# Kernel optimization log

Measured on AMD Instinct MI355X. Metric: run time of the kernel, lower is better.

The kernel has to match this reference:

```python
import jax, jax.numpy as jnp
import numpy as np
from math import sqrt

B, L, S, H, E = 4, 2048, 2048, 8, 64
T = 1.0  # softmax temperature


def setup_inputs() -> dict:
    key = jax.random.key(0)
    kq, kk, kv = jax.random.split(key, 3)
    q = jax.random.normal(kq, (B, L, H, E), dtype=jnp.float32)
    k = jax.random.normal(kk, (B, S, H, E), dtype=jnp.float32)
    v = jax.random.normal(kv, (B, S, H, E), dtype=jnp.float32)
    mask = jnp.zeros((B, L), dtype=jnp.bool_)  # unused by the module, kept for signature fidelity
    return {"q": q, "k": k, "v": v, "mask": mask}


def reference(q, k, v, mask):
    Bq, Lq, Hq, Eq = q.shape
    # [B,L,H,E] -> [B,H,E,L]; FFT over time axis
    xq = jnp.transpose(q, (0, 2, 3, 1))
    xk = jnp.transpose(k, (0, 2, 3, 1))
    xv = jnpp_t = jnp.transpose(v, (0, 2, 3, 1))
    xq_ft = jnp.fft.rfft(xq, axis=-1, norm='ortho')   # [B,H,E,Lf]
    xk_ft = jnp.fft.rfft(xk, axis=-1, norm='ortho')   # [B,H,E,Sf]
    xv_ft = jnp.fft.rfft(xv, axis=-1, norm='ortho')   # [B,H,E,Sf]
    # complex frequency-domain scores [B,H,Lf,Sf]
    scores = jnp.einsum('bhex,bhey->bhxy', xq_ft, jnp.conj(xk_ft)) / sqrt(Eq)
    # activation == 'softmax': softmax over |scores|/T, then real-weighted complex mix
    attn = jax.nn.softmax(jnp.abs(scores) / T, axis=-1)
    xqkv_ft = jnp.einsum('bhxy,bhey->bhex', attn.astype(xv_ft.dtype), xv_ft)  # [B,H,E,Lf]
    out = jnp.fft.irfft(xqkv_ft, n=Lq, axis=-1, norm='ortho')  # [B,H,E,L]
    return jnp.transpose(out, (0, 3, 1, 2))  # [B,L,H,E]
```

## Files before the change

kernel.cpp:

```cpp
#include <hip/hip_runtime.h>
#include <hip/hip_bf16.h>
#include <math.h>

#define LOGN  11
#define NN    2048
#define LOGM  10
#define MM    1024
#define NF    1025
#define NYP   1056
#define TWO_PI 6.283185307179586f
#define INV_SQRT_N 0.022097086912079608f
#define INV_SCALE  0.044194173824159216f
#define LOG2E      1.4426950408889634f

#define PAD(i) ((i) + ((i) >> 4))
#define MMP   1088
#define TWP   816

typedef __attribute__((ext_vector_type(8))) short bhalf8;
typedef __attribute__((ext_vector_type(4))) float f32x4;

#define MFMA16(a, b, c) __builtin_amdgcn_mfma_f32_16x16x32_bf16(a, b, c, 0, 0, 0)

#define GLD16(gp, lp)                                                              \
    __builtin_amdgcn_global_load_lds(                                              \
        (const __attribute__((address_space(1))) void*)(gp),                       \
        (__attribute__((address_space(3))) void*)(lp), 16, 0, 0)

#define CVTPK(dst, lo, hi) \
    asm("v_cvt_pk_bf16_f32 %0, %1, %2" : "=v"(dst) : "v"(lo), "v"(hi))

#define EXP2F(dst, src) \
    asm("v_exp_f32 %0, %1" : "=v"(dst) : "v"(src))

__device__ __forceinline__ unsigned short f2bf(float f) {
    union { float f; unsigned u; } v; v.f = f;
    unsigned r = v.u + 0x7FFFu + ((v.u >> 16) & 1u);
    return (unsigned short)(r >> 16);
}
__device__ __forceinline__ float bf2f(unsigned short h) {
    union { unsigned u; float f; } v; v.u = ((unsigned)h) << 16;
    return v.f;
}

__device__ __forceinline__ int dr4_10(unsigned j) {
    unsigned r = __brev(j) >> 22;
    return (int)(((r & 0x155u) << 1) | ((r >> 1) & 0x155u));
}

__global__ __launch_bounds__(256) void mk_tables(float2* __restrict__ twf,
                                                 float2* __restrict__ twi,
                                                 float2* __restrict__ rc)
{
    int i = blockIdx.x * 256 + threadIdx.x;
    if (i < 768) {
        float ang = TWO_PI * (float)i / (float)MM;
        float sv, cv;
        __sincosf(ang, &sv, &cv);
        twf[i] = make_float2(cv, -sv);
        twi[i] = make_float2(cv,  sv);
    }
    if (i < 1025) {
        float ang = TWO_PI * (float)i / (float)NN;
        float sv, cv;
        __sincosf(ang, &sv, &cv);
        rc[i] = make_float2(cv, sv);
    }
}

template<bool FWD>
__device__ __forceinline__ void fft_r4_1024(float2* buf, const float2* tw, int tid)
{
    {
        int i0 = tid * 4;
        int q0 = PAD(i0), q1 = PAD(i0 + 1), q2 = PAD(i0 + 2), q3 = PAD(i0 + 3);
        float2 a = buf[q0], b = buf[q1], c = buf[q2], d = buf[q3];
        float2 apc = make_float2(a.x + c.x, a.y + c.y);
        float2 amc = make_float2(a.x - c.x, a.y - c.y);
        float2 bpd = make_float2(b.x + d.x, b.y + d.y);
        float2 bmd = make_float2(b.x - d.x, b.y - d.y);
        buf[q0] = make_float2(apc.x + bpd.x, apc.y + bpd.y);
        buf[q2] = make_float2(apc.x - bpd.x, apc.y - bpd.y);
        if (FWD) {
            buf[q1] = make_float2(amc.x + bmd.y, amc.y - bmd.x);
            buf[q3] = make_float2(amc.x - bmd.y, amc.y + bmd.x);
        } else {
            buf[q1] = make_float2(amc.x - bmd.y, amc.y + bmd.x);
            buf[q3] = make_float2(amc.x + bmd.y, amc.y - bmd.x);
        }
        __syncthreads();
    }
    #pragma unroll
    for (int s = 1; s < 5; s++) {
        int L  = 1 << (2 * s);
        int p  = tid & (L - 1);
        int i0 = ((tid >> (2 * s)) << (2 * s + 2)) + p;
        int e  = p << (8 - 2 * s);
        float2 w1 = tw[PAD(e)], w2 = tw[PAD(2 * e)], w3 = tw[PAD(3 * e)];
        int q0 = PAD(i0), q1 = PAD(i0 + L), q2 = PAD(i0 + 2 * L), q3 = PAD(i0 + 3 * L);
        float2 a  = buf[q0];
        float2 xb = buf[q1], xc = buf[q2], xd = buf[q3];
        float2 b = make_float2(xb.x * w1.x - xb.y * w1.y, xb.x * w1.y + xb.y * w1.x);
        float2 c = make_float2(xc.x * w2.x - xc.y * w2.y, xc.x * w2.y + xc.y * w2.x);
        float2 d = make_float2(xd.x * w3.x - xd.y * w3.y, xd.x * w3.y + xd.y * w3.x);
        float2 apc = make_float2(a.x + c.x, a.y + c.y);
        float2 amc = make_float2(a.x - c.x, a.y - c.y);
        float2 bpd = make_float2(b.x + d.x, b.y + d.y);
        float2 bmd = make_float2(b.x - d.x, b.y - d.y);
        buf[q0] = make_float2(apc.x + bpd.x, apc.y + bpd.y);
        buf[q2] = make_float2(apc.x - bpd.x, apc.y - bpd.y);
        if (FWD) {
            buf[q1] = make_float2(amc.x + bmd.y, amc.y - bmd.x);
            buf[q3] = make_float2(amc.x - bmd.y, amc.y + bmd.x);
        } else {
            buf[q1] = make_float2(amc.x - bmd.y, amc.y + bmd.x);
            buf[q3] = make_float2(amc.x + bmd.y, amc.y - bmd.x);
        }
        __syncthreads();
    }
}

__global__ __launch_bounds__(256) void tr_fwd(const float* __restrict__ q,
                                              const float* __restrict__ k,
                                              const float* __restrict__ v,
                                              unsigned short* __restrict__ ttr)
{
    __shared__ float Ts[64][65];
    int tt     = blockIdx.x;
    int h      = blockIdx.y;
    int z      = blockIdx.z;
    int tensor = z >> 2;
    int b      = z & 3;
    int tid    = threadIdx.x;
    int t0     = tt * 64;

    const float* in = (tensor == 0) ? q : (tensor == 1) ? k : v;

    {
        int tl = tid >> 2, ec = (tid & 3) * 16;
        const float* src = in + ((size_t)b * 2048 + t0 + tl) * 512 + h * 64 + ec;
        #pragma unroll
        for (int m = 0; m < 4; m++) {
            float4 v4 = *(const float4*)(src + m * 4);
            Ts[tl][ec + m * 4 + 0] = v4.x;
            Ts[tl][ec + m * 4 + 1] = v4.y;
            Ts[tl][ec + m * 4 + 2] = v4.z;
            Ts[tl][ec + m * 4 + 3] = v4.w;
        }
    }
    __syncthreads();
    {
        int el = tid >> 2, tc = (tid & 3) * 16;
        size_t row = ((size_t)(tensor * 32 + b * 8 + h)) * 64 + el;
        unsigned short* dst = ttr + row * 2048 + t0 + tc;
        #pragma unroll
        for (int m = 0; m < 4; m++) {
            float a0 = Ts[tc + m * 4 + 0][el], a1 = Ts[tc + m * 4 + 1][el];
            float a2 = Ts[tc + m * 4 + 2][el], a3 = Ts[tc + m * 4 + 3][el];
            unsigned u0, u1;
            CVTPK(u0, a0, a1);
            CVTPK(u1, a2, a3);
            uint2 o; o.x = u0; o.y = u1;
            *(uint2*)(dst + m * 4) = o;
        }
    }
}

__global__ __launch_bounds__(256) void fft_fwd(const unsigned short* __restrict__ ttr,
                                               const float2* __restrict__ twg,
                                               const float2* __restrict__ rc,
                                               unsigned short* __restrict__ Pq,
                                               unsigned short* __restrict__ Pk,
                                               unsigned short* __restrict__ Pv)
{
    __shared__ float2 buf[MMP];
    __shared__ float2 tw[TWP];

    int g      = blockIdx.x;
    int p      = g % 96;
    int e      = g / 96;
    int tensor = p / 32;
    int bh     = p % 32;
    int tid    = threadIdx.x;

    unsigned short* plane = (tensor == 0) ? Pq : (tensor == 1) ? Pk : Pv;
    float scl = (tensor == 0) ? (INV_SQRT_N * 0.125f * LOG2E) : INV_SQRT_N;
    int vk3 = (tensor == 2) ? (((e >> 2) & 3) << 3) : 0;

    #pragma unroll
    for (int i = tid; i < 768; i += 256) tw[PAD(i)] = twg[i];

    const unsigned short* src = ttr + ((size_t)p * 64 + e) * 2048;
    #pragma unroll
    for (int i = 0; i < 4; i++) {
        int j = tid + 256 * i;
        unsigned pr = *(const unsigned*)(src + 2 * j);
        float x0 = bf2f((unsigned short)(pr & 0xFFFFu));
        float x1 = bf2f((unsigned short)(pr >> 16));
        buf[PAD(dr4_10((unsigned)j))] = make_float2(x0, x1);
    }
    __syncthreads();

    fft_r4_1024<true>(buf, tw, tid);

    unsigned short* dre = plane + ((size_t)bh * 128 + e) * NYP;
    unsigned short* dim_ = dre + (size_t)64 * NYP;

#define RPOINT(Ai, Bi, CX, CY, XR, XI) do {                                \
        float Ex = 0.5f * (Ai.x + Bi.x), Ey = 0.5f * (Ai.y - Bi.y);        \
        float Dx = 0.5f * (Ai.x - Bi.x), Dy = 0.5f * (Ai.y + Bi.y);        \
        float Ox = Dy, Oy = -Dx;                                           \
        XR = (Ex + (CX) * Ox + (CY) * Oy) * scl;                           \
        XI = (Ey + (CX) * Oy - (CY) * Ox) * scl;                           \
    } while (0)

    #pragma unroll
    for (int i = 0; i < 2; i++) {
        int kk = 2 * tid + 512 * i;
        float2 A0 = buf[PAD(kk)];
        float2 B0 = buf[PAD((MM - kk) & (MM - 1))];
        float2 A1 = buf[PAD(kk + 1)];
        float2 B1 = buf[PAD(MM - kk - 1)];
        float4 rq = *(const float4*)(&rc[kk]);
        float Xr0, Xi0, Xr1, Xi1;
        RPOINT(A0, B0, rq.x, rq.y, Xr0, Xi0);
        RPOINT(A1, B1, rq.z, rq.w, Xr1, Xi1);
        unsigned ur, ui;
        CVTPK(ur, Xr0, Xr1);
        CVTPK(ui, Xi0, Xi1);
        int ks = kk ^ vk3;
        *(unsigned*)(dre + ks)  = ur;
        *(unsigned*)(dim_ + ks) = ui;
    }
    if (tid < 16) {
        unsigned ur = 0, ui = 0;
        if (tid == 0) {
            float2 A = buf[PAD(0)];
            float Xr = (A.x - A.y) * scl;
            float zz = 0.f;
            CVTPK(ur, Xr, zz);
        }
        int ks = (1024 + 2 * tid) ^ vk3;
        *(unsigned*)(dre + ks)  = ur;
        *(unsigned*)(dim_ + ks) = ui;
    }
#undef RPOINT
}

__global__ __launch_bounds__(256) void qkpack(const unsigned short* __restrict__ Pq,
                                              const unsigned short* __restrict__ Pk,
                                              unsigned short* __restrict__ Qp,
                                              unsigned short* __restrict__ Kp)
{
    __shared__ unsigned short Ts[32][136];
    int y0  = blockIdx.x * 32;
    int bh  = blockIdx.y;
    int tsr = blockIdx.z;
    int tid = threadIdx.x;

    const unsigned short* srcp = (tsr == 0) ? Pq : Pk;
    unsigned short* dstp       = (tsr == 0) ? Qp : Kp;

    {
        int kk = tid >> 1, seg = tid & 1;
        const unsigned short* sp = srcp + ((size_t)bh * 128 + kk) * NYP + y0 + seg * 16;
        uint4 va = *(const uint4*)sp;
        uint4 vb = *(const uint4*)(sp + 8);
        const unsigned short* pa = (const unsigned short*)&va;
        const unsigned short* pb = (const unsigned short*)&vb;
        #pragma unroll
        for (int j = 0; j < 8; j++) Ts[seg * 16 + j][kk] = pa[j];
        #pragma unroll
        for (int j = 0; j < 8; j++) Ts[seg * 16 + 8 + j][kk] = pb[j];
    }
    __syncthreads();
    {
        int y = tid >> 3, c = tid & 7;
        uint4 lo = *(const uint4*)&Ts[y][c * 16];
        uint4 hi = *(const uint4*)&Ts[y][c * 16 + 8];
        char* rowb = (char*)(dstp + ((size_t)bh * NYP + y0 + y) * 128);
        if (tsr == 0) {
            *(uint4*)(rowb + c * 32)      = lo;
            *(uint4*)(rowb + c * 32 + 16) = hi;
        } else {
            int s = y & 7;
            *(uint4*)(rowb + (((2 * c)     ^ s) << 4)) = lo;
            *(uint4*)(rowb + (((2 * c + 1) ^ s) << 4)) = hi;
        }
    }
}

struct FlashShared {
    union {
        struct {
            unsigned short Ks[2][32][128];
            unsigned short Vs[2][128][32];
        } kv;
        unsigned short OutT[128][72];
    } u;
    unsigned short Ps[4][16][40];
};

template<int NH>
__global__ __launch_bounds__(256) void flash_mfma(
    const unsigned short* __restrict__ Qp,
    const unsigned short* __restrict__ Kp,
    const unsigned short* __restrict__ Vt,
    unsigned short* __restrict__ nb0,
    unsigned short* __restrict__ nb1,
    float* __restrict__ lbuf)
{
    __shared__ FlashShared S;

    int g    = blockIdx.x;
    int bh   = g & 31;
    int idx  = g >> 5;
    int half = idx / 17;
    int x0   = (idx % 17) * 64;
    int tid  = threadIdx.x;
    int w    = tid >> 6;
    int lane = tid & 63;
    int qd   = lane >> 4;
    int col  = lane & 15;

    int xrow = x0 + w * 16 + col;
    int xq   = min(xrow, 1024);
    const unsigned short* qb = Qp + ((size_t)bh * NYP + xq) * 128 + qd * 8;
    bhalf8 Are[4], Aim[4];
    #pragma unroll
    for (int ks = 0; ks < 4; ks++) Are[ks] = *(const bhalf8*)(qb + ks * 32);
    Aim[0] = Are[2];
    Aim[1] = Are[3];
    #pragma unroll
    for (int ks = 0; ks < 2; ks++) {
        bhalf8 t = Are[ks];
        unsigned* u = (unsigned*)&t;
        #pragma unroll
        for (int j = 0; j < 4; j++) u[j] ^= 0x80008000u;
        Aim[ks + 2] = t;
    }

    f32x4 O[8];
    #pragma unroll
    for (int n = 0; n < 8; n++) O[n] = (f32x4){0.f, 0.f, 0.f, 0.f};
    float Lacc[4] = {0.f, 0.f, 0.f, 0.f};

    int yt0 = (half * 33) / NH, yt1 = ((half + 1) * 33) / NH;

    const char* ksrc = (const char*)Kp
        + ((size_t)bh * NYP + (size_t)yt0 * 32 + w * 8) * 256 + lane * 16;
    const char* vbase = (const char*)Vt + (size_t)bh * 128 * (NYP * 2);
    const char* vsrc0 = vbase + ((size_t)(w * 32) + (lane >> 2)) * (NYP * 2)
                        + (size_t)yt0 * 64 + (lane & 3) * 16;
    const char* vsrc1 = vsrc0 + (size_t)16 * (NYP * 2);

    int sw = col & 7;
    int kco[4];
    #pragma unroll
    for (int ks = 0; ks < 4; ks++) kco[ks] = ((ks * 4 + qd) ^ sw) * 8;
    int vq = (qd ^ ((col >> 2) & 3)) * 8;

    {
        int pb = yt0 & 1;
        GLD16(ksrc,         &S.u.kv.Ks[pb][w * 8][0]);
        GLD16(ksrc + 1024,  &S.u.kv.Ks[pb][w * 8 + 4][0]);
        GLD16(vsrc0,        &S.u.kv.Vs[pb][w * 32][0]);
        GLD16(vsrc1,        &S.u.kv.Vs[pb][w * 32 + 16][0]);
        ksrc += 8192; vsrc0 += 64; vsrc1 += 64;
    }

    for (int yt = yt0; yt < yt1; yt++) {
        int cb = yt & 1, nb = cb ^ 1;
        if (yt + 1 < yt1) {
            GLD16(ksrc,         &S.u.kv.Ks[nb][w * 8][0]);
            GLD16(ksrc + 1024,  &S.u.kv.Ks[nb][w * 8 + 4][0]);
            GLD16(vsrc0,        &S.u.kv.Vs[nb][w * 32][0]);
            GLD16(vsrc1,        &S.u.kv.Vs[nb][w * 32 + 16][0]);
            ksrc += 8192; vsrc0 += 64; vsrc1 += 64;
            __builtin_amdgcn_sched_barrier(0);
            asm volatile("s_waitcnt vmcnt(4)" ::: "memory");
        } else {
            __builtin_amdgcn_sched_barrier(0);
            asm volatile("s_waitcnt vmcnt(0)" ::: "memory");
        }
        __builtin_amdgcn_sched_barrier(0);
        __builtin_amdgcn_s_barrier();
        __builtin_amdgcn_sched_barrier(0);

        const unsigned short* k0 = &S.u.kv.Ks[cb][col][0];
        const unsigned short* k1 = &S.u.kv.Ks[cb][col + 16][0];

        f32x4 sre[2], sim[2];
        #pragma unroll
        for (int sc = 0; sc < 2; sc++) {
            sre[sc] = (f32x4){0.f, 0.f, 0.f, 0.f};
            sim[sc] = (f32x4){0.f, 0.f, 0.f, 0.f};
        }
        __builtin_amdgcn_s_setprio(1);
        #pragma unroll
        for (int ks = 0; ks < 4; ks++) {
            bhalf8 b0 = *(const bhalf8*)(k0 + kco[ks]);
            bhalf8 b1 = *(const bhalf8*)(k1 + kco[ks]);
            sre[0] = MFMA16(Are[ks], b0, sre[0]);
            sim[0] = MFMA16(Aim[ks], b0, sim[0]);
            sre[1] = MFMA16(Are[ks], b1, sre[1]);
            sim[1] = MFMA16(Aim[ks], b1, sim[1]);
        }
        __builtin_amdgcn_s_setprio(0);

        #pragma unroll
        for (int r = 0; r < 4; r++) {
            float re0 = sre[0][r], im0 = sim[0][r];
            float re1 = sre[1][r], im1 = sim[1][r];
            float s0 = __builtin_amdgcn_sqrtf(fmaf(re0, re0, im0 * im0));
            float s1 = __builtin_amdgcn_sqrtf(fmaf(re1, re1, im1 * im1));
            float p0, p1;
            EXP2F(p0, s0);
            EXP2F(p1, s1);
            Lacc[r] += p0 + p1;
            unsigned up;
            CVTPK(up, p0, p1);
            S.Ps[w][qd * 4 + r][col]      = (unsigned short)up;
            S.Ps[w][qd * 4 + r][col + 16] = (unsigned short)(up >> 16);
        }

        bhalf8 pa = *(const bhalf8*)&S.Ps[w][col][qd * 8];
        __builtin_amdgcn_s_setprio(1);
        #pragma unroll
        for (int n = 0; n < 8; n++) {
            bhalf8 bv = *(const bhalf8*)&S.u.kv.Vs[cb][n * 16 + col][vq];
            O[n] = MFMA16(pa, bv, O[n]);
        }
        __builtin_amdgcn_s_setprio(0);

        asm volatile("s_waitcnt lgkmcnt(0)" ::: "memory");
        __builtin_amdgcn_sched_barrier(0);
        __builtin_amdgcn_s_barrier();
        __builtin_amdgcn_sched_barrier(0);
    }

    #pragma unroll
    for (int r = 0; r < 4; r++) {
        float ls = Lacc[r];
        ls += __shfl_xor(ls, 1);
        ls += __shfl_xor(ls, 2);
        ls += __shfl_xor(ls, 4);
        ls += __shfl_xor(ls, 8);
        if (yt1 == 33) ls -= 31.0f;
        int x = x0 + w * 16 + qd * 4 + r;
        if (x <= 1024 && col == 0)
            lbuf[((size_t)half * 32 + bh) * NYP + x] = ls;
    }

    const size_t HSZ = (size_t)32 * 128 * NYP;
    unsigned short* nplane = (half < 2 ? nb0 : nb1) + (size_t)(half & 1) * HSZ;

    __syncthreads();
    #pragma unroll
    for (int n = 0; n < 8; n++) {
        unsigned u0, u1;
        CVTPK(u0, O[n][0], O[n][1]);
        CVTPK(u1, O[n][2], O[n][3]);
        *(unsigned*)&S.u.OutT[n * 16 + col][w * 16 + qd * 4]     = u0;
        *(unsigned*)&S.u.OutT[n * 16 + col][w * 16 + qd * 4 + 2] = u1;
    }
    __syncthreads();
    {
        int kk2 = tid >> 1, seg = tid & 1;
        int xg  = x0 + seg * 32;
        if (xg < NYP) {
            unsigned short* dst = nplane + ((size_t)bh * 128 + kk2) * NYP + xg;
            const unsigned short* srcl = &S.u.OutT[kk2][seg * 32];
            #pragma unroll
            for (int m = 0; m < 4; m++)
                *(uint4*)(dst + m * 8) = *(const uint4*)(srcl + m * 8);
        }
    }
}

template<int NH>
__global__ __launch_bounds__(256) void fft_inv(const unsigned short* __restrict__ nb0,
                                               const unsigned short* __restrict__ nb1,
                                               const float2* __restrict__ twg,
                                               const float2* __restrict__ rc,
                                               const float* __restrict__ lbuf,
                                               float* __restrict__ st)
{
    __shared__ float2 buf[MMP];
    __shared__ float2 tw[TWP];

    int s   = blockIdx.x;
    int e   = s & 63;
    int bh  = s >> 6;
    int tid = threadIdx.x;

    #pragma unroll
    for (int i = tid; i < 768; i += 256) tw[PAD(i)] = twg[i];

    const size_t HSZ = (size_t)32 * 128 * NYP;
    const unsigned short* pre[NH];
    const unsigned short* pim[NH];
    const float* lb[NH];
    #pragma unroll
    for (int h = 0; h < NH; h++) {
        const unsigned short* base = (h < 2 ? nb0 : nb1) + (size_t)(h & 1) * HSZ;
        pre[h] = base + ((size_t)bh * 128 + e) * NYP;
        pim[h] = base + ((size_t)bh * 128 + 64 + e) * NYP;
        lb[h]  = lbuf + ((size_t)h * 32 + bh) * NYP;
    }

    #pragma unroll
    for (int i = 0; i < 4; i++) {
        int kk = tid + 256 * i;
        int x1 = kk, x2 = 1024 - kk;
        float d1 = 0.f, d2 = 0.f;
        float Axs = 0.f, Ays = 0.f, Bxs = 0.f, Bys = 0.f;
        #pragma unroll
        for (int h = 0; h < NH; h++) {
            d1 += lb[h][x1];
            d2 += lb[h][x2];
            Axs += bf2f(pre[h][x1]);
            Ays += bf2f(pim[h][x1]);
            Bxs += bf2f(pre[h][x2]);
            Bys += bf2f(pim[h][x2]);
        }
        float iv1 = 1.f / d1, iv2 = 1.f / d2;
        float Ax = Axs * iv1, Ay = Ays * iv1;
        float Bx = Bxs * iv2, By = -(Bys * iv2);
        float Ex = 0.5f * (Ax + Bx), Ey = 0.5f * (Ay + By);
        float Dx = 0.5f * (Ax - Bx), Dy = 0.5f * (Ay - By);
        float2 rcv = rc[kk];
        float Ox = Dx * rcv.x - Dy * rcv.y;
        float Oy = Dx * rcv.y + Dy * rcv.x;
        buf[PAD(dr4_10((unsigned)kk))] = make_float2(Ex - Oy, Ey + Ox);
    }
    __syncthreads();

    fft_r4_1024<false>(buf, tw, tid);

    float* dst = st + ((size_t)bh * 64 + e) * 2048;
    #pragma unroll
    for (int i = 0; i < 4; i++) {
        int j = tid + 256 * i;
        float2 z = buf[PAD(j)];
        *(float2*)&dst[2 * j] = make_float2(z.x * INV_SCALE, z.y * INV_SCALE);
    }
}

__global__ __launch_bounds__(256) void out_tr(const float* __restrict__ st,
                                              float* __restrict__ out)
{
    __shared__ float Ts[64][65];
    int tt  = blockIdx.x;
    int h   = blockIdx.y;
    int b   = blockIdx.z;
    int tid = threadIdx.x;
    int bh  = b * 8 + h;

    {
        int e = tid >> 2, tc = (tid & 3) * 16;
        const float* src = st + ((size_t)bh * 64 + e) * 2048 + tt * 64 + tc;
        #pragma unroll
        for (int m = 0; m < 4; m++) {
            float4 v4 = *(const float4*)(src + m * 4);
            Ts[e][tc + m * 4 + 0] = v4.x;
            Ts[e][tc + m * 4 + 1] = v4.y;
            Ts[e][tc + m * 4 + 2] = v4.z;
            Ts[e][tc + m * 4 + 3] = v4.w;
        }
    }
    __syncthreads();
    {
        int t = tid >> 2, ec = (tid & 3) * 16;
        float* dst = out + (size_t)b * 2048 * 512 + (size_t)(tt * 64 + t) * 512
                     + h * 64 + ec;
        #pragma unroll
        for (int m = 0; m < 4; m++) {
            float4 v4;
            v4.x = Ts[ec + m * 4 + 0][t];
            v4.y = Ts[ec + m * 4 + 1][t];
            v4.z = Ts[ec + m * 4 + 2][t];
            v4.w = Ts[ec + m * 4 + 3][t];
            *(float4*)(dst + m * 4) = v4;
        }
    }
}

extern "C" void kernel_launch(void* const* d_in, const int* in_sizes, int n_in,
                              void* d_out, int out_size, void* d_ws, size_t ws_size,
                              hipStream_t stream)
{
    const float* q = (const float*)d_in[0];
    const float* k = (const float*)d_in[1];
    const float* v = (const float*)d_in[2];
    float* out = (float*)d_out;

    char* ws = (char*)d_ws;
    const size_t PL = (size_t)32 * 128 * NYP * sizeof(unsigned short);
    unsigned short* Pq = (unsigned short*)(ws);
    unsigned short* Pk = (unsigned short*)(ws + PL);
    unsigned short* Pv = (unsigned short*)(ws + 2 * PL);
    unsigned short* ttr = (unsigned short*)(ws + 3 * PL);
    unsigned short* Qp = (unsigned short*)(ws + 3 * PL);
    unsigned short* Kp = (unsigned short*)(ws + 4 * PL);
    float* st = (float*)(ws + 3 * PL);

    const size_t lbuf4 = (size_t)4 * 32 * NYP * sizeof(float);
    const size_t lbuf2 = (size_t)2 * 32 * NYP * sizeof(float);
    const size_t TBL   = (size_t)(768 + 768 + 1025) * sizeof(float2);
    bool big = ws_size >= 7 * PL + lbuf4 + TBL;

    char* tb = big ? (ws + 7 * PL + lbuf4) : (ws + 5 * PL + lbuf2);
    float2* twf = (float2*)tb;
    float2* twi = twf + 768;
    float2* rc  = twi + 768;

    hipLaunchKernelGGL(mk_tables, dim3(5), dim3(256), 0, stream, twf, twi, rc);
    hipLaunchKernelGGL(tr_fwd, dim3(32, 8, 12), dim3(256), 0, stream,
                       q, k, v, ttr);
    hipLaunchKernelGGL(fft_fwd, dim3(3 * 2048), dim3(256), 0, stream,
                       ttr, twf, rc, Pq, Pk, Pv);
    hipLaunchKernelGGL(qkpack, dim3(33, 32, 2), dim3(256), 0, stream,
                       Pq, Pk, Qp, Kp);

    if (big) {
        unsigned short* nb0 = (unsigned short*)(ws);
        unsigned short* nb1 = (unsigned short*)(ws + 5 * PL);
        float* lbuf = (float*)(ws + 7 * PL);
        hipLaunchKernelGGL((flash_mfma<4>), dim3(17 * 4 * 32), dim3(256), 0, stream,
                           Qp, Kp, Pv, nb0, nb1, lbuf);
        hipLaunchKernelGGL((fft_inv<4>), dim3(2048), dim3(256), 0, stream,
                           nb0, nb1, twi, rc, lbuf, st);
    } else {
        unsigned short* nb0 = (unsigned short*)(ws);
        float* lbuf = (float*)(ws + 5 * PL);
        hipLaunchKernelGGL((flash_mfma<2>), dim3(17 * 2 * 32), dim3(256), 0, stream,
                           Qp, Kp, Pv, nb0, nb0, lbuf);
        hipLaunchKernelGGL((fft_inv<2>), dim3(2048), dim3(256), 0, stream,
                           nb0, nb0, twi, rc, lbuf, st);
    }

    hipLaunchKernelGGL(out_tr, dim3(32, 8, 4), dim3(256), 0, stream,
                       st, out);
}
```

Baseline: 197.7 us.

## Batch two FFT rows per block and fold table generation into transpose kernel

The forward and inverse FFT kernels now process two rows per 256-thread block, sharing twiddle loads, index math and barriers across both rows and halving the grid size. In the inverse kernel the softmax denominator sums are reused across the two rows. Twiddle table generation moves into the first few blocks of tr_fwd, which removes one kernel launch. The cost is double the shared memory per block, which may reduce occupancy, plus more registers.

```diff
diff --git a/kernel.cpp b/kernel.cpp
--- a/kernel.cpp
+++ b/kernel.cpp
@@ -48,45 +48,29 @@
     return (int)(((r & 0x155u) << 1) | ((r >> 1) & 0x155u));
 }
 
-__global__ __launch_bounds__(256) void mk_tables(float2* __restrict__ twf,
-                                                 float2* __restrict__ twi,
-                                                 float2* __restrict__ rc)
-{
-    int i = blockIdx.x * 256 + threadIdx.x;
-    if (i < 768) {
-        float ang = TWO_PI * (float)i / (float)MM;
-        float sv, cv;
-        __sincosf(ang, &sv, &cv);
-        twf[i] = make_float2(cv, -sv);
-        twi[i] = make_float2(cv,  sv);
-    }
-    if (i < 1025) {
-        float ang = TWO_PI * (float)i / (float)NN;
-        float sv, cv;
-        __sincosf(ang, &sv, &cv);
-        rc[i] = make_float2(cv, sv);
-    }
-}
-
 template<bool FWD>
-__device__ __forceinline__ void fft_r4_1024(float2* buf, const float2* tw, int tid)
+__device__ __forceinline__ void fft_r4_1024x2(float2 buf[2][MMP],
+                                              const float2* tw, int tid)
 {
     {
         int i0 = tid * 4;
         int q0 = PAD(i0), q1 = PAD(i0 + 1), q2 = PAD(i0 + 2), q3 = PAD(i0 + 3);
-        float2 a = buf[q0], b = buf[q1], c = buf[q2], d = buf[q3];
-        float2 apc = make_float2(a.x + c.x, a.y + c.y);
-        float2 amc = make_float2(a.x - c.x, a.y - c.y);
-        float2 bpd = make_float2(b.x + d.x, b.y + d.y);
-        float2 bmd = make_float2(b.x - d.x, b.y - d.y);
-        buf[q0] = make_float2(apc.x + bpd.x, apc.y + bpd.y);
-        buf[q2] = make_float2(apc.x - bpd.x, apc.y - bpd.y);
-        if (FWD) {
-            buf[q1] = make_float2(amc.x + bmd.y, amc.y - bmd.x);
-            buf[q3] = make_float2(amc.x - bmd.y, amc.y + bmd.x);
-        } else {
-            buf[q1] = make_float2(amc.x - bmd.y, amc.y + bmd.x);
-            buf[q3] = make_float2(amc.x + bmd.y, amc.y - bmd.x);
+        #pragma unroll
+        for (int b2 = 0; b2 < 2; b2++) {
+            float2 a = buf[b2][q0], b = buf[b2][q1], c = buf[b2][q2], d = buf[b2][q3];
+            float2 apc = make_float2(a.x + c.x, a.y + c.y);
+            float2 amc = make_float2(a.x - c.x, a.y - c.y);
+            float2 bpd = make_float2(b.x + d.x, b.y + d.y);
+            float2 bmd = make_float2(b.x - d.x, b.y - d.y);
+            buf[b2][q0] = make_float2(apc.x + bpd.x, apc.y + bpd.y);
+            buf[b2][q2] = make_float2(apc.x - bpd.x, apc.y - bpd.y);
+            if (FWD) {
+                buf[b2][q1] = make_float2(amc.x + bmd.y, amc.y - bmd.x);
+                buf[b2][q3] = make_float2(amc.x - bmd.y, amc.y + bmd.x);
+            } else {
+                buf[b2][q1] = make_float2(amc.x - bmd.y, amc.y + bmd.x);
+                buf[b2][q3] = make_float2(amc.x + bmd.y, amc.y - bmd.x);
+            }
         }
         __syncthreads();
     }
@@ -98,23 +82,26 @@
         int e  = p << (8 - 2 * s);
         float2 w1 = tw[PAD(e)], w2 = tw[PAD(2 * e)], w3 = tw[PAD(3 * e)];
         int q0 = PAD(i0), q1 = PAD(i0 + L), q2 = PAD(i0 + 2 * L), q3 = PAD(i0 + 3 * L);
-        float2 a  = buf[q0];
-        float2 xb = buf[q1], xc = buf[q2], xd = buf[q3];
-        float2 b = make_float2(xb.x * w1.x - xb.y * w1.y, xb.x * w1.y + xb.y * w1.x);
-        float2 c = make_float2(xc.x * w2.x - xc.y * w2.y, xc.x * w2.y + xc.y * w2.x);
-        float2 d = make_float2(xd.x * w3.x - xd.y * w3.y, xd.x * w3.y + xd.y * w3.x);
-        float2 apc = make_float2(a.x + c.x, a.y + c.y);
-        float2 amc = make_float2(a.x - c.x, a.y - c.y);
-        float2 bpd = make_float2(b.x + d.x, b.y + d.y);
-        float2 bmd = make_float2(b.x - d.x, b.y - d.y);
-        buf[q0] = make_float2(apc.x + bpd.x, apc.y + bpd.y);
-        buf[q2] = make_float2(apc.x - bpd.x, apc.y - bpd.y);
-        if (FWD) {
-            buf[q1] = make_float2(amc.x + bmd.y, amc.y - bmd.x);
-            buf[q3] = make_float2(amc.x - bmd.y, amc.y + bmd.x);
-        } else {
-            buf[q1] = make_float2(amc.x - bmd.y, amc.y + bmd.x);
-            buf[q3] = make_float2(amc.x + bmd.y, amc.y - bmd.x);
+        #pragma unroll
+        for (int b2 = 0; b2 < 2; b2++) {
+            float2 a  = buf[b2][q0];
+            float2 xb = buf[b2][q1], xc = buf[b2][q2], xd = buf[b2][q3];
+            float2 b = make_float2(xb.x * w1.x - xb.y * w1.y, xb.x * w1.y + xb.y * w1.x);
+            float2 c = make_float2(xc.x * w2.x - xc.y * w2.y, xc.x * w2.y + xc.y * w2.x);
+            float2 d = make_float2(xd.x * w3.x - xd.y * w3.y, xd.x * w3.y + xd.y * w3.x);
+            float2 apc = make_float2(a.x + c.x, a.y + c.y);
+            float2 amc = make_float2(a.x - c.x, a.y - c.y);
+            float2 bpd = make_float2(b.x + d.x, b.y + d.y);
+            float2 bmd = make_float2(b.x - d.x, b.y - d.y);
+            buf[b2][q0] = make_float2(apc.x + bpd.x, apc.y + bpd.y);
+            buf[b2][q2] = make_float2(apc.x - bpd.x, apc.y - bpd.y);
+            if (FWD) {
+                buf[b2][q1] = make_float2(amc.x + bmd.y, amc.y - bmd.x);
+                buf[b2][q3] = make_float2(amc.x - bmd.y, amc.y + bmd.x);
+            } else {
+                buf[b2][q1] = make_float2(amc.x - bmd.y, amc.y + bmd.x);
+                buf[b2][q3] = make_float2(amc.x + bmd.y, amc.y - bmd.x);
+            }
         }
         __syncthreads();
     }
@@ -123,7 +110,10 @@
 __global__ __launch_bounds__(256) void tr_fwd(const float* __restrict__ q,
                                               const float* __restrict__ k,
                                               const float* __restrict__ v,
-                                              unsigned short* __restrict__ ttr)
+                                              unsigned short* __restrict__ ttr,
+                                              float2* __restrict__ twf,
+                                              float2* __restrict__ twi,
+                                              float2* __restrict__ rc)
 {
     __shared__ float Ts[64][65];
     int tt     = blockIdx.x;
@@ -134,6 +124,23 @@
     int tid    = threadIdx.x;
     int t0     = tt * 64;
 
+    if (z == 0 && h == 0 && tt < 5) {
+        int i = tt * 256 + tid;
+        if (i < 768) {
+            float ang = TWO_PI * (float)i / (float)MM;
+            float sv, cv;
+            __sincosf(ang, &sv, &cv);
+            twf[i] = make_float2(cv, -sv);
+            twi[i] = make_float2(cv,  sv);
+        }
+        if (i < 1025) {
+            float ang = TWO_PI * (float)i / (float)NN;
+            float sv, cv;
+            __sincosf(ang, &sv, &cv);
+            rc[i] = make_float2(cv, sv);
+        }
+    }
+
     const float* in = (tensor == 0) ? q : (tensor == 1) ? k : v;
 
     {
@@ -173,76 +180,94 @@
                                                unsigned short* __restrict__ Pk,
                                                unsigned short* __restrict__ Pv)
 {
-    __shared__ float2 buf[MMP];
+    __shared__ float2 buf[2][MMP];
     __shared__ float2 tw[TWP];
 
-    int g      = blockIdx.x;
-    int p      = g % 96;
-    int e      = g / 96;
-    int tensor = p / 32;
-    int bh     = p % 32;
-    int tid    = threadIdx.x;
-
-    unsigned short* plane = (tensor == 0) ? Pq : (tensor == 1) ? Pk : Pv;
-    float scl = (tensor == 0) ? (INV_SQRT_N * 0.125f * LOG2E) : INV_SQRT_N;
-    int vk3 = (tensor == 2) ? (((e >> 2) & 3) << 3) : 0;
+    int g   = blockIdx.x;
+    int tid = threadIdx.x;
+
+    float scl[2];
+    int vk3[2];
+    unsigned short* dre[2];
+    unsigned short* dim_[2];
+    const unsigned short* src[2];
+    #pragma unroll
+    for (int b2 = 0; b2 < 2; b2++) {
+        int s      = 2 * g + b2;
+        int p      = s % 96;
+        int e      = s / 96;
+        int tensor = p / 32;
+        int bh     = p % 32;
+        unsigned short* plane = (tensor == 0) ? Pq : (tensor == 1) ? Pk : Pv;
+        scl[b2] = (tensor == 0) ? (INV_SQRT_N * 0.125f * LOG2E) : INV_SQRT_N;
+        vk3[b2] = (tensor == 2) ? (((e >> 2) & 3) << 3) : 0;
+        dre[b2] = plane + ((size_t)bh * 128 + e) * NYP;
+        dim_[b2] = dre[b2] + (size_t)64 * NYP;
+        src[b2] = ttr + ((size_t)p * 64 + e) * 2048;
+    }
 
     #pragma unroll
     for (int i = tid; i < 768; i += 256) tw[PAD(i)] = twg[i];
 
-    const unsigned short* src = ttr + ((size_t)p * 64 + e) * 2048;
     #pragma unroll
     for (int i = 0; i < 4; i++) {
         int j = tid + 256 * i;
-        unsigned pr = *(const unsigned*)(src + 2 * j);
-        float x0 = bf2f((unsigned short)(pr & 0xFFFFu));
-        float x1 = bf2f((unsigned short)(pr >> 16));
-        buf[PAD(dr4_10((unsigned)j))] = make_float2(x0, x1);
+        int d = PAD(dr4_10((unsigned)j));
+        #pragma unroll
+        for (int b2 = 0; b2 < 2; b2++) {
+            unsigned pr = *(const unsigned*)(src[b2] + 2 * j);
+            float x0 = bf2f((unsigned short)(pr & 0xFFFFu));
+            float x1 = bf2f((unsigned short)(pr >> 16));
+            buf[b2][d] = make_float2(x0, x1);
+        }
     }
     __syncthreads();
 
-    fft_r4_1024<true>(buf, tw, tid);
-
-    unsigned short* dre = plane + ((size_t)bh * 128 + e) * NYP;
-    unsigned short* dim_ = dre + (size_t)64 * NYP;
-
-#define RPOINT(Ai, Bi, CX, CY, XR, XI) do {                                \
+    fft_r4_1024x2<true>(buf, tw, tid);
+
+#define RPOINT(Ai, Bi, CX, CY, SCL, XR, XI) do {                           \
         float Ex = 0.5f * (Ai.x + Bi.x), Ey = 0.5f * (Ai.y - Bi.y);        \
         float Dx = 0.5f * (Ai.x - Bi.x), Dy = 0.5f * (Ai.y + Bi.y);        \
         float Ox = Dy, Oy = -Dx;                                           \
-        XR = (Ex + (CX) * Ox + (CY) * Oy) * scl;                           \
-        XI = (Ey + (CX) * Oy - (CY) * Ox) * scl;                           \
+        XR = (Ex + (CX) * Ox + (CY) * Oy) * (SCL);                         \
+        XI = (Ey + (CX) * Oy - (CY) * Ox) * (SCL);                         \
     } while (0)
 
     #pragma unroll
     for (int i = 0; i < 2; i++) {
         int kk = 2 * tid + 512 * i;
-        float2 A0 = buf[PAD(kk)];
-        float2 B0 = buf[PAD((MM - kk) & (MM - 1))];
-        float2 A1 = buf[PAD(kk + 1)];
-        float2 B1 = buf[PAD(MM - kk - 1)];
+        int d0 = PAD(kk), d0c = PAD((MM - kk) & (MM - 1));
+        int d1 = PAD(kk + 1), d1c = PAD(MM - kk - 1);
         float4 rq = *(const float4*)(&rc[kk]);
-        float Xr0, Xi0, Xr1, Xi1;
-        RPOINT(A0, B0, rq.x, rq.y, Xr0, Xi0);
-        RPOINT(A1, B1, rq.z, rq.w, Xr1, Xi1);
-        unsigned ur, ui;
-        CVTPK(ur, Xr0, Xr1);
-        CVTPK(ui, Xi0, Xi1);
-        int ks = kk ^ vk3;
-        *(unsigned*)(dre + ks)  = ur;
-        *(unsigned*)(dim_ + ks) = ui;
+        #pragma unroll
+        for (int b2 = 0; b2 < 2; b2++) {
+            float2 A0 = buf[b2][d0], B0 = buf[b2][d0c];
+            float2 A1 = buf[b2][d1], B1 = buf[b2][d1c];
+            float Xr0, Xi0, Xr1, Xi1;
+            RPOINT(A0, B0, rq.x, rq.y, scl[b2], Xr0, Xi0);
+            RPOINT(A1, B1, rq.z, rq.w, scl[b2], Xr1, Xi1);
+            unsigned ur, ui;
+            CVTPK(ur, Xr0, Xr1);
+            CVTPK(ui, Xi0, Xi1);
+            int ks = kk ^ vk3[b2];
+            *(unsigned*)(dre[b2] + ks)  = ur;
+            *(unsigned*)(dim_[b2] + ks) = ui;
+        }
     }
     if (tid < 16) {
-        unsigned ur = 0, ui = 0;
-        if (tid == 0) {
-            float2 A = buf[PAD(0)];
-            float Xr = (A.x - A.y) * scl;
-            float zz = 0.f;
-            CVTPK(ur, Xr, zz);
-        }
-        int ks = (1024 + 2 * tid) ^ vk3;
-        *(unsigned*)(dre + ks)  = ur;
-        *(unsigned*)(dim_ + ks) = ui;
+        #pragma unroll
+        for (int b2 = 0; b2 < 2; b2++) {
+            unsigned ur = 0, ui = 0;
+            if (tid == 0) {
+                float2 A = buf[b2][PAD(0)];
+                float Xr = (A.x - A.y) * scl[b2];
+                float zz = 0.f;
+                CVTPK(ur, Xr, zz);
+            }
+            int ks = (1024 + 2 * tid) ^ vk3[b2];
+            *(unsigned*)(dre[b2] + ks)  = ur;
+            *(unsigned*)(dim_[b2] + ks) = ui;
+        }
     }
 #undef RPOINT
 }
@@ -486,12 +511,12 @@
                                                const float* __restrict__ lbuf,
                                                float* __restrict__ st)
 {
-    __shared__ float2 buf[MMP];
+    __shared__ float2 buf[2][MMP];
     __shared__ float2 tw[TWP];
 
-    int s   = blockIdx.x;
-    int e   = s & 63;
-    int bh  = s >> 6;
+    int g   = blockIdx.x;
+    int e   = (2 * g) & 63;
+    int bh  = (2 * g) >> 6;
     int tid = threadIdx.x;
 
     #pragma unroll
@@ -514,36 +539,47 @@
         int kk = tid + 256 * i;
         int x1 = kk, x2 = 1024 - kk;
         float d1 = 0.f, d2 = 0.f;
-        float Axs = 0.f, Ays = 0.f, Bxs = 0.f, Bys = 0.f;
         #pragma unroll
         for (int h = 0; h < NH; h++) {
             d1 += lb[h][x1];
             d2 += lb[h][x2];
-            Axs += bf2f(pre[h][x1]);
-            Ays += bf2f(pim[h][x1]);
-            Bxs += bf2f(pre[h][x2]);
-            Bys += bf2f(pim[h][x2]);
         }
         float iv1 = 1.f / d1, iv2 = 1.f / d2;
-        float Ax = Axs * iv1, Ay = Ays * iv1;
-        float Bx = Bxs * iv2, By = -(Bys * iv2);
-        float Ex = 0.5f * (Ax + Bx), Ey = 0.5f * (Ay + By);
-        float Dx = 0.5f * (Ax - Bx), Dy = 0.5f * (Ay - By);
         float2 rcv = rc[kk];
-        float Ox = Dx * rcv.x - Dy * rcv.y;
-        float Oy = Dx * rcv.y + Dy * rcv.x;
-        buf[PAD(dr4_10((unsigned)kk))] = make_float2(Ex - Oy, Ey + Ox);
+        int dd = PAD(dr4_10((unsigned)kk));
+        #pragma unroll
+        for (int b2 = 0; b2 < 2; b2++) {
+            int off = b2 * NYP;
+            float Axs = 0.f, Ays = 0.f, Bxs = 0.f, Bys = 0.f;
+            #pragma unroll
+            for (int h = 0; h < NH; h++) {
+                Axs += bf2f(pre[h][off + x1]);
+                Ays += bf2f(pim[h][off + x1]);
+                Bxs += bf2f(pre[h][off + x2]);
+                Bys += bf2f(pim[h][off + x2]);
+            }
+            float Ax = Axs * iv1, Ay = Ays * iv1;
+            float Bx = Bxs * iv2, By = -(Bys * iv2);
+            float Ex = 0.5f * (Ax + Bx), Ey = 0.5f * (Ay + By);
+            float Dx = 0.5f * (Ax - Bx), Dy = 0.5f * (Ay - By);
+            float Ox = Dx * rcv.x - Dy * rcv.y;
+            float Oy = Dx * rcv.y + Dy * rcv.x;
+            buf[b2][dd] = make_float2(Ex - Oy, Ey + Ox);
+        }
     }
     __syncthreads();
 
-    fft_r4_1024<false>(buf, tw, tid);
+    fft_r4_1024x2<false>(buf, tw, tid);
 
     float* dst = st + ((size_t)bh * 64 + e) * 2048;
     #pragma unroll
     for (int i = 0; i < 4; i++) {
         int j = tid + 256 * i;
-        float2 z = buf[PAD(j)];
-        *(float2*)&dst[2 * j] = make_float2(z.x * INV_SCALE, z.y * INV_SCALE);
+        int dj = PAD(j);
+        float2 z0 = buf[0][dj];
+        float2 z1 = buf[1][dj];
+        *(float2*)&dst[2 * j] = make_float2(z0.x * INV_SCALE, z0.y * INV_SCALE);
+        *(float2*)&dst[2048 + 2 * j] = make_float2(z1.x * INV_SCALE, z1.y * INV_SCALE);
     }
 }
 
@@ -615,10 +651,9 @@
     float2* twi = twf + 768;
     float2* rc  = twi + 768;
 
-    hipLaunchKernelGGL(mk_tables, dim3(5), dim3(256), 0, stream, twf, twi, rc);
     hipLaunchKernelGGL(tr_fwd, dim3(32, 8, 12), dim3(256), 0, stream,
-                       q, k, v, ttr);
-    hipLaunchKernelGGL(fft_fwd, dim3(3 * 2048), dim3(256), 0, stream,
+                       q, k, v, ttr, twf, twi, rc);
+    hipLaunchKernelGGL(fft_fwd, dim3(3 * 1024), dim3(256), 0, stream,
                        ttr, twf, rc, Pq, Pk, Pv);
     hipLaunchKernelGGL(qkpack, dim3(33, 32, 2), dim3(256), 0, stream,
                        Pq, Pk, Qp, Kp);
@@ -629,14 +664,14 @@
         float* lbuf = (float*)(ws + 7 * PL);
         hipLaunchKernelGGL((flash_mfma<4>), dim3(17 * 4 * 32), dim3(256), 0, stream,
                            Qp, Kp, Pv, nb0, nb1, lbuf);
-        hipLaunchKernelGGL((fft_inv<4>), dim3(2048), dim3(256), 0, stream,
+        hipLaunchKernelGGL((fft_inv<4>), dim3(1024), dim3(256), 0, stream,
                            nb0, nb1, twi, rc, lbuf, st);
     } else {
         unsigned short* nb0 = (unsigned short*)(ws);
         float* lbuf = (float*)(ws + 5 * PL);
         hipLaunchKernelGGL((flash_mfma<2>), dim3(17 * 2 * 32), dim3(256), 0, stream,
                            Qp, Kp, Pv, nb0, nb0, lbuf);
-        hipLaunchKernelGGL((fft_inv<2>), dim3(2048), dim3(256), 0, stream,
+        hipLaunchKernelGGL((fft_inv<2>), dim3(1024), dim3(256), 0, stream,
                            nb0, nb0, twi, rc, lbuf, st);
     }
 
```

Result: no change. 197.1 us (-0.3%).

## Restructure FFT kernels to one wave per transform with register-resident radix-16 stages

Applied to the files above, without the earlier changes.

Rewrites the forward and inverse 1024-point FFTs so a 64-thread wave owns one transform. Each thread holds 16 points in registers and does the first two radix-4 stages there, leaving two LDS stages, which cuts the number of block-wide barriers and LDS round trips. Blocks now hold two transforms of 128 threads each. The twiddle-table setup kernel is folded into tr_fwd to remove one launch. The risks are higher register pressure and a new data permutation that has to match the old bit-reversed ordering.

```diff
diff --git a/kernel.cpp b/kernel.cpp
--- a/kernel.cpp
+++ b/kernel.cpp
@@ -43,87 +43,104 @@
     return v.f;
 }
 
-__device__ __forceinline__ int dr4_10(unsigned j) {
-    unsigned r = __brev(j) >> 22;
-    return (int)(((r & 0x155u) << 1) | ((r >> 1) & 0x155u));
-}
-
-__global__ __launch_bounds__(256) void mk_tables(float2* __restrict__ twf,
-                                                 float2* __restrict__ twi,
-                                                 float2* __restrict__ rc)
-{
-    int i = blockIdx.x * 256 + threadIdx.x;
-    if (i < 768) {
-        float ang = TWO_PI * (float)i / (float)MM;
-        float sv, cv;
-        __sincosf(ang, &sv, &cv);
-        twf[i] = make_float2(cv, -sv);
-        twi[i] = make_float2(cv,  sv);
-    }
-    if (i < 1025) {
-        float ang = TWO_PI * (float)i / (float)NN;
-        float sv, cv;
-        __sincosf(ang, &sv, &cv);
-        rc[i] = make_float2(cv, sv);
-    }
+__device__ __forceinline__ float2 cmul(float2 x, float2 w) {
+    return make_float2(x.x * w.x - x.y * w.y, x.x * w.y + x.y * w.x);
 }
 
 template<bool FWD>
-__device__ __forceinline__ void fft_r4_1024(float2* buf, const float2* tw, int tid)
-{
-    {
-        int i0 = tid * 4;
-        int q0 = PAD(i0), q1 = PAD(i0 + 1), q2 = PAD(i0 + 2), q3 = PAD(i0 + 3);
-        float2 a = buf[q0], b = buf[q1], c = buf[q2], d = buf[q3];
-        float2 apc = make_float2(a.x + c.x, a.y + c.y);
-        float2 amc = make_float2(a.x - c.x, a.y - c.y);
-        float2 bpd = make_float2(b.x + d.x, b.y + d.y);
-        float2 bmd = make_float2(b.x - d.x, b.y - d.y);
-        buf[q0] = make_float2(apc.x + bpd.x, apc.y + bpd.y);
-        buf[q2] = make_float2(apc.x - bpd.x, apc.y - bpd.y);
-        if (FWD) {
-            buf[q1] = make_float2(amc.x + bmd.y, amc.y - bmd.x);
-            buf[q3] = make_float2(amc.x - bmd.y, amc.y + bmd.x);
-        } else {
-            buf[q1] = make_float2(amc.x - bmd.y, amc.y + bmd.x);
-            buf[q3] = make_float2(amc.x + bmd.y, amc.y - bmd.x);
-        }
-        __syncthreads();
-    }
-    #pragma unroll
-    for (int s = 1; s < 5; s++) {
-        int L  = 1 << (2 * s);
-        int p  = tid & (L - 1);
-        int i0 = ((tid >> (2 * s)) << (2 * s + 2)) + p;
-        int e  = p << (8 - 2 * s);
-        float2 w1 = tw[PAD(e)], w2 = tw[PAD(2 * e)], w3 = tw[PAD(3 * e)];
-        int q0 = PAD(i0), q1 = PAD(i0 + L), q2 = PAD(i0 + 2 * L), q3 = PAD(i0 + 3 * L);
-        float2 a  = buf[q0];
-        float2 xb = buf[q1], xc = buf[q2], xd = buf[q3];
-        float2 b = make_float2(xb.x * w1.x - xb.y * w1.y, xb.x * w1.y + xb.y * w1.x);
-        float2 c = make_float2(xc.x * w2.x - xc.y * w2.y, xc.x * w2.y + xc.y * w2.x);
-        float2 d = make_float2(xd.x * w3.x - xd.y * w3.y, xd.x * w3.y + xd.y * w3.x);
-        float2 apc = make_float2(a.x + c.x, a.y + c.y);
-        float2 amc = make_float2(a.x - c.x, a.y - c.y);
-        float2 bpd = make_float2(b.x + d.x, b.y + d.y);
-        float2 bmd = make_float2(b.x - d.x, b.y - d.y);
-        buf[q0] = make_float2(apc.x + bpd.x, apc.y + bpd.y);
-        buf[q2] = make_float2(apc.x - bpd.x, apc.y - bpd.y);
-        if (FWD) {
-            buf[q1] = make_float2(amc.x + bmd.y, amc.y - bmd.x);
-            buf[q3] = make_float2(amc.x - bmd.y, amc.y + bmd.x);
-        } else {
-            buf[q1] = make_float2(amc.x - bmd.y, amc.y + bmd.x);
-            buf[q3] = make_float2(amc.x + bmd.y, amc.y - bmd.x);
-        }
-        __syncthreads();
-    }
+__device__ __forceinline__ void r4(float2& a, float2& b, float2& c, float2& d) {
+    float2 apc = make_float2(a.x + c.x, a.y + c.y);
+    float2 amc = make_float2(a.x - c.x, a.y - c.y);
+    float2 bpd = make_float2(b.x + d.x, b.y + d.y);
+    float2 bmd = make_float2(b.x - d.x, b.y - d.y);
+    a = make_float2(apc.x + bpd.x, apc.y + bpd.y);
+    c = make_float2(apc.x - bpd.x, apc.y - bpd.y);
+    if (FWD) {
+        b = make_float2(amc.x + bmd.y, amc.y - bmd.x);
+        d = make_float2(amc.x - bmd.y, amc.y + bmd.x);
+    } else {
+        b = make_float2(amc.x - bmd.y, amc.y + bmd.x);
+        d = make_float2(amc.x + bmd.y, amc.y - bmd.x);
+    }
+}
+
+template<bool FWD>
+__device__ __forceinline__ void s0s1(float2 x[16], const float2* tw) {
+    #pragma unroll
+    for (int c = 0; c < 4; c++)
+        r4<FWD>(x[c], x[4 + c], x[8 + c], x[12 + c]);
+    #pragma unroll
+    for (int i = 0; i < 4; i++) {
+        float2 w1 = tw[PAD(64 * i)], w2 = tw[PAD(128 * i)], w3 = tw[PAD(192 * i)];
+        x[4 * i + 1] = cmul(x[4 * i + 1], w1);
+        x[4 * i + 2] = cmul(x[4 * i + 2], w2);
+        x[4 * i + 3] = cmul(x[4 * i + 3], w3);
+        r4<FWD>(x[4 * i], x[4 * i + 1], x[4 * i + 2], x[4 * i + 3]);
+    }
+}
+
+template<bool FWD>
+__device__ __forceinline__ void fft_mid(float2* bufS, const float2* tw, int q, int r)
+{
+    {
+        float2 v[4][4];
+        #pragma unroll
+        for (int d = 0; d < 4; d++)
+            #pragma unroll
+            for (int c = 0; c < 4; c++)
+                v[d][c] = bufS[PAD(256 * q + 64 * d + 16 * c + r)];
+        float2 w1 = tw[PAD(16 * r)], w2 = tw[PAD(32 * r)], w3 = tw[PAD(48 * r)];
+        #pragma unroll
+        for (int d = 0; d < 4; d++) {
+            v[d][1] = cmul(v[d][1], w1);
+            v[d][2] = cmul(v[d][2], w2);
+            v[d][3] = cmul(v[d][3], w3);
+            r4<FWD>(v[d][0], v[d][1], v[d][2], v[d][3]);
+        }
+        #pragma unroll
+        for (int c = 0; c < 4; c++) {
+            int e = 4 * (16 * c + r);
+            float2 u1 = tw[PAD(e)], u2 = tw[PAD(2 * e)], u3 = tw[PAD(3 * e)];
+            v[1][c] = cmul(v[1][c], u1);
+            v[2][c] = cmul(v[2][c], u2);
+            v[3][c] = cmul(v[3][c], u3);
+            r4<FWD>(v[0][c], v[1][c], v[2][c], v[3][c]);
+        }
+        #pragma unroll
+        for (int d = 0; d < 4; d++)
+            #pragma unroll
+            for (int c = 0; c < 4; c++)
+                bufS[PAD(256 * q + 64 * d + 16 * c + r)] = v[d][c];
+    }
+    __syncthreads();
+    {
+        #pragma unroll
+        for (int k = 0; k < 4; k++) {
+            int p4 = 16 * q + r + 64 * k;
+            float2 a = bufS[PAD(p4)];
+            float2 b = bufS[PAD(p4 + 256)];
+            float2 c = bufS[PAD(p4 + 512)];
+            float2 d = bufS[PAD(p4 + 768)];
+            b = cmul(b, tw[PAD(p4)]);
+            c = cmul(c, tw[PAD(2 * p4)]);
+            d = cmul(d, tw[PAD(3 * p4)]);
+            r4<FWD>(a, b, c, d);
+            bufS[PAD(p4)]       = a;
+            bufS[PAD(p4 + 256)] = b;
+            bufS[PAD(p4 + 512)] = c;
+            bufS[PAD(p4 + 768)] = d;
+        }
+    }
+    __syncthreads();
 }
 
 __global__ __launch_bounds__(256) void tr_fwd(const float* __restrict__ q,
                                               const float* __restrict__ k,
                                               const float* __restrict__ v,
-                                              unsigned short* __restrict__ ttr)
+                                              unsigned short* __restrict__ ttr,
+                                              float2* __restrict__ twf,
+                                              float2* __restrict__ twi,
+                                              float2* __restrict__ rc)
 {
     __shared__ float Ts[64][65];
     int tt     = blockIdx.x;
@@ -134,6 +151,23 @@
     int tid    = threadIdx.x;
     int t0     = tt * 64;
 
+    if (z == 0 && h == 0 && tt < 5) {
+        int i = tt * 256 + tid;
+        if (i < 768) {
+            float ang = TWO_PI * (float)i / (float)MM;
+            float sv, cv;
+            __sincosf(ang, &sv, &cv);
+            twf[i] = make_float2(cv, -sv);
+            twi[i] = make_float2(cv,  sv);
+        }
+        if (i < 1025) {
+            float ang = TWO_PI * (float)i / (float)NN;
+            float sv, cv;
+            __sincosf(ang, &sv, &cv);
+            rc[i] = make_float2(cv, sv);
+        }
+    }
+
     const float* in = (tensor == 0) ? q : (tensor == 1) ? k : v;
 
     {
@@ -166,45 +200,54 @@
     }
 }
 
-__global__ __launch_bounds__(256) void fft_fwd(const unsigned short* __restrict__ ttr,
+__global__ __launch_bounds__(128) void fft_fwd(const unsigned short* __restrict__ ttr,
                                                const float2* __restrict__ twg,
                                                const float2* __restrict__ rc,
                                                unsigned short* __restrict__ Pq,
                                                unsigned short* __restrict__ Pk,
                                                unsigned short* __restrict__ Pv)
 {
-    __shared__ float2 buf[MMP];
+    __shared__ float2 buf[2][MMP];
     __shared__ float2 tw[TWP];
 
-    int g      = blockIdx.x;
-    int p      = g % 96;
-    int e      = g / 96;
+    int g  = blockIdx.x;
+    int t  = threadIdx.x;
+    int w  = t >> 6, tp = t & 63;
+    int q4 = tp >> 4, r = tp & 15;
+    int G  = ((tp & 3) << 4) | (tp & 12) | (tp >> 4);
+
+    int s      = 2 * g + w;
+    int p      = s % 96;
+    int e      = s / 96;
     int tensor = p / 32;
     int bh     = p % 32;
-    int tid    = threadIdx.x;
 
     unsigned short* plane = (tensor == 0) ? Pq : (tensor == 1) ? Pk : Pv;
     float scl = (tensor == 0) ? (INV_SQRT_N * 0.125f * LOG2E) : INV_SQRT_N;
     int vk3 = (tensor == 2) ? (((e >> 2) & 3) << 3) : 0;
-
-    #pragma unroll
-    for (int i = tid; i < 768; i += 256) tw[PAD(i)] = twg[i];
-
+    unsigned short* dre  = plane + ((size_t)bh * 128 + e) * NYP;
+    unsigned short* dim_ = dre + (size_t)64 * NYP;
     const unsigned short* src = ttr + ((size_t)p * 64 + e) * 2048;
-    #pragma unroll
-    for (int i = 0; i < 4; i++) {
-        int j = tid + 256 * i;
-        unsigned pr = *(const unsigned*)(src + 2 * j);
-        float x0 = bf2f((unsigned short)(pr & 0xFFFFu));
-        float x1 = bf2f((unsigned short)(pr >> 16));
-        buf[PAD(dr4_10((unsigned)j))] = make_float2(x0, x1);
-    }
-    __syncthreads();
-
-    fft_r4_1024<true>(buf, tw, tid);
-
-    unsigned short* dre = plane + ((size_t)bh * 128 + e) * NYP;
-    unsigned short* dim_ = dre + (size_t)64 * NYP;
+
+    #pragma unroll
+    for (int i = t; i < 768; i += 128) tw[PAD(i)] = twg[i];
+
+    float2* bufS = buf[w];
+
+    float2 x[16];
+    #pragma unroll
+    for (int k = 0; k < 16; k++) {
+        unsigned pr = *(const unsigned*)(src + 2 * (tp + 64 * k));
+        x[k] = make_float2(bf2f((unsigned short)(pr & 0xFFFFu)),
+                           bf2f((unsigned short)(pr >> 16)));
+    }
+    s0s1<true>(x, tw);
+    #pragma unroll
+    for (int k = 0; k < 16; k++)
+        bufS[PAD(16 * G + 4 * (k & 3) + (k >> 2))] = x[k];
+    __syncthreads();
+
+    fft_mid<true>(bufS, tw, q4, r);
 
 #define RPOINT(Ai, Bi, CX, CY, XR, XI) do {                                \
         float Ex = 0.5f * (Ai.x + Bi.x), Ey = 0.5f * (Ai.y - Bi.y);        \
@@ -215,12 +258,12 @@
     } while (0)
 
     #pragma unroll
-    for (int i = 0; i < 2; i++) {
-        int kk = 2 * tid + 512 * i;
-        float2 A0 = buf[PAD(kk)];
-        float2 B0 = buf[PAD((MM - kk) & (MM - 1))];
-        float2 A1 = buf[PAD(kk + 1)];
-        float2 B1 = buf[PAD(MM - kk - 1)];
+    for (int i = 0; i < 8; i++) {
+        int kk = 2 * tp + 128 * i;
+        float2 A0 = bufS[PAD(kk)];
+        float2 B0 = bufS[PAD((MM - kk) & (MM - 1))];
+        float2 A1 = bufS[PAD(kk + 1)];
+        float2 B1 = bufS[PAD(MM - kk - 1)];
         float4 rq = *(const float4*)(&rc[kk]);
         float Xr0, Xi0, Xr1, Xi1;
         RPOINT(A0, B0, rq.x, rq.y, Xr0, Xi0);
@@ -232,15 +275,15 @@
         *(unsigned*)(dre + ks)  = ur;
         *(unsigned*)(dim_ + ks) = ui;
     }
-    if (tid < 16) {
+    if (tp < 16) {
         unsigned ur = 0, ui = 0;
-        if (tid == 0) {
-            float2 A = buf[PAD(0)];
+        if (tp == 0) {
+            float2 A = bufS[PAD(0)];
             float Xr = (A.x - A.y) * scl;
             float zz = 0.f;
             CVTPK(ur, Xr, zz);
         }
-        int ks = (1024 + 2 * tid) ^ vk3;
+        int ks = (1024 + 2 * tp) ^ vk3;
         *(unsigned*)(dre + ks)  = ur;
         *(unsigned*)(dim_ + ks) = ui;
     }
@@ -479,23 +522,28 @@
 }
 
 template<int NH>
-__global__ __launch_bounds__(256) void fft_inv(const unsigned short* __restrict__ nb0,
+__global__ __launch_bounds__(128) void fft_inv(const unsigned short* __restrict__ nb0,
                                                const unsigned short* __restrict__ nb1,
                                                const float2* __restrict__ twg,
                                                const float2* __restrict__ rc,
                                                const float* __restrict__ lbuf,
                                                float* __restrict__ st)
 {
-    __shared__ float2 buf[MMP];
+    __shared__ float2 buf[2][MMP];
     __shared__ float2 tw[TWP];
 
-    int s   = blockIdx.x;
-    int e   = s & 63;
-    int bh  = s >> 6;
-    int tid = threadIdx.x;
-
-    #pragma unroll
-    for (int i = tid; i < 768; i += 256) tw[PAD(i)] = twg[i];
+    int g  = blockIdx.x;
+    int t  = threadIdx.x;
+    int w  = t >> 6, tp = t & 63;
+    int q4 = tp >> 4, r = tp & 15;
+    int G  = ((tp & 3) << 4) | (tp & 12) | (tp >> 4);
+
+    int sidx = 2 * g + w;
+    int e    = sidx & 63;
+    int bh   = sidx >> 6;
+
+    #pragma unroll
+    for (int i = t; i < 768; i += 128) tw[PAD(i)] = twg[i];
 
     const size_t HSZ = (size_t)32 * 128 * NYP;
     const unsigned short* pre[NH];
@@ -509,9 +557,12 @@
         lb[h]  = lbuf + ((size_t)h * 32 + bh) * NYP;
     }
 
-    #pragma unroll
-    for (int i = 0; i < 4; i++) {
-        int kk = tid + 256 * i;
+    float2* bufS = buf[w];
+
+    float2 x[16];
+    #pragma unroll
+    for (int k = 0; k < 16; k++) {
+        int kk = tp + 64 * k;
         int x1 = kk, x2 = 1024 - kk;
         float d1 = 0.f, d2 = 0.f;
         float Axs = 0.f, Ays = 0.f, Bxs = 0.f, Bys = 0.f;
@@ -532,17 +583,21 @@
         float2 rcv = rc[kk];
         float Ox = Dx * rcv.x - Dy * rcv.y;
         float Oy = Dx * rcv.y + Dy * rcv.x;
-        buf[PAD(dr4_10((unsigned)kk))] = make_float2(Ex - Oy, Ey + Ox);
-    }
-    __syncthreads();
-
-    fft_r4_1024<false>(buf, tw, tid);
+        x[k] = make_float2(Ex - Oy, Ey + Ox);
+    }
+    s0s1<false>(x, tw);
+    #pragma unroll
+    for (int k = 0; k < 16; k++)
+        bufS[PAD(16 * G + 4 * (k & 3) + (k >> 2))] = x[k];
+    __syncthreads();
+
+    fft_mid<false>(bufS, tw, q4, r);
 
     float* dst = st + ((size_t)bh * 64 + e) * 2048;
     #pragma unroll
-    for (int i = 0; i < 4; i++) {
-        int j = tid + 256 * i;
-        float2 z = buf[PAD(j)];
+    for (int i = 0; i < 16; i++) {
+        int j = tp + 64 * i;
+        float2 z = bufS[PAD(j)];
         *(float2*)&dst[2 * j] = make_float2(z.x * INV_SCALE, z.y * INV_SCALE);
     }
 }
@@ -615,10 +670,9 @@
     float2* twi = twf + 768;
     float2* rc  = twi + 768;
 
-    hipLaunchKernelGGL(mk_tables, dim3(5), dim3(256), 0, stream, twf, twi, rc);
     hipLaunchKernelGGL(tr_fwd, dim3(32, 8, 12), dim3(256), 0, stream,
-                       q, k, v, ttr);
-    hipLaunchKernelGGL(fft_fwd, dim3(3 * 2048), dim3(256), 0, stream,
+                       q, k, v, ttr, twf, twi, rc);
+    hipLaunchKernelGGL(fft_fwd, dim3(3 * 1024), dim3(128), 0, stream,
                        ttr, twf, rc, Pq, Pk, Pv);
     hipLaunchKernelGGL(qkpack, dim3(33, 32, 2), dim3(256), 0, stream,
                        Pq, Pk, Qp, Kp);
@@ -629,14 +683,14 @@
         float* lbuf = (float*)(ws + 7 * PL);
         hipLaunchKernelGGL((flash_mfma<4>), dim3(17 * 4 * 32), dim3(256), 0, stream,
                            Qp, Kp, Pv, nb0, nb1, lbuf);
-        hipLaunchKernelGGL((fft_inv<4>), dim3(2048), dim3(256), 0, stream,
+        hipLaunchKernelGGL((fft_inv<4>), dim3(1024), dim3(128), 0, stream,
                            nb0, nb1, twi, rc, lbuf, st);
     } else {
         unsigned short* nb0 = (unsigned short*)(ws);
         float* lbuf = (float*)(ws + 5 * PL);
         hipLaunchKernelGGL((flash_mfma<2>), dim3(17 * 2 * 32), dim3(256), 0, stream,
                            Qp, Kp, Pv, nb0, nb0, lbuf);
-        hipLaunchKernelGGL((fft_inv<2>), dim3(2048), dim3(256), 0, stream,
+        hipLaunchKernelGGL((fft_inv<2>), dim3(1024), dim3(128), 0, stream,
                            nb0, nb0, twi, rc, lbuf, st);
     }
 
```

New measurement: 197.9 us. Within noise of the previous version (+0.1%).
